# Performance work log

Hardware: AMD Instinct MI355X
Metric: run time of the kernel (lower is better)

The kernel has to match this reference:

```python
import jax, jax.numpy as jnp
import numpy as np

B, S, E = 1, 2048, 2048
H, KVH, D = 16, 4, 128  # query heads, kv heads, head dim (emb_kq == emb_v == 128)
SPLITS = (H * D, KVH * D, KVH * D)  # fused qkv output split sizes


def _rope_tables(seq_len, dim, base=10000.0):
    inv_freq = 1.0 / (base ** (jnp.arange(0, dim, 2, dtype=jnp.float32) / dim))
    t = jnp.arange(seq_len, dtype=jnp.float32)
    freqs = jnp.outer(t, inv_freq)  # [S, D/2]
    emb = jnp.concatenate([freqs, freqs], axis=-1)  # [S, D]
    return jnp.cos(emb), jnp.sin(emb)


def _rotate_half(x):
    x1, x2 = jnp.split(x, 2, axis=-1)
    return jnp.concatenate([-x2, x1], axis=-1)


def _apply_rope(x, cos, sin):
    # x: [B, S, h, D]; cos/sin: [S, D]
    c = cos[None, :, None, :]
    s = sin[None, :, None, :]
    return x * c + _rotate_half(x) * s


def setup_inputs() -> dict:
    key = jax.random.key(0)
    k1, k2, k3 = jax.random.split(key, 3)
    x = jax.random.normal(k1, (B, S, E), dtype=jnp.float32)
    w_qkv = jax.random.normal(k2, (sum(SPLITS), E), dtype=jnp.float32) * 0.02
    w_dense = jax.random.normal(k3, (E, H * D), dtype=jnp.float32) * 0.02
    return {"x": x, "w_qkv": w_qkv, "w_dense": w_dense}


def reference(x, w_qkv, w_dense):
    # fused QKV projection: [B, S, sum(SPLITS)]
    qkv = jnp.einsum("bse,fe->bsf", x, w_qkv)
    q, k, v = jnp.split(qkv, np.cumsum(SPLITS)[:-1].tolist(), axis=-1)
    q = q.reshape(B, S, H, D)
    k = k.reshape(B, S, KVH, D)
    v = v.reshape(B, S, KVH, D)

    # rotary position encoding on q, k
    cos, sin = _rope_tables(S, D)
    q = _apply_rope(q, cos, sin)
    k = _apply_rope(k, cos, sin)

    # GQA: expand kv heads to match query heads
    rep = H // KVH
    k = jnp.repeat(k, rep, axis=2)  # [B, S, H, D]
    v = jnp.repeat(v, rep, axis=2)

    # SDPA, causal
    scale = 1.0 / jnp.sqrt(jnp.asarray(D, dtype=x.dtype))
    scores = jnp.einsum("bqhd,bkhd->bhqk", q, k) * scale
    causal = jnp.tril(jnp.ones((S, S), dtype=bool))
    scores = jnp.where(causal[None, None], scores, jnp.asarray(-jnp.inf, scores.dtype))
    attn = jax.nn.softmax(scores, axis=-1)
    ctx = jnp.einsum("bhqk,bkhd->bqhd", attn, v).reshape(B, S, H * D)

    # output projection
    return jnp.einsum("bsf,ef->bse", ctx, w_dense)
```

## Files before the change

kernel.cpp:

```cpp
#include <hip/hip_runtime.h>
#include <hip/hip_bf16.h>
#include <math.h>

typedef __bf16 bf16;
typedef __bf16 bf16x4 __attribute__((ext_vector_type(4)));
typedef __bf16 bf16x8 __attribute__((ext_vector_type(8)));
typedef float  f32x4  __attribute__((ext_vector_type(4)));
typedef float  f32x16 __attribute__((ext_vector_type(16)));

#define S_LEN 2048
#define EMB   2048
#define NH    16
#define NKV   4
#define HD    128
#define FQKV  3072

__device__ __forceinline__ f32x4 mfma16(bf16x8 a, bf16x8 b, f32x4 c) {
  return __builtin_amdgcn_mfma_f32_16x16x32_bf16(a, b, c, 0, 0, 0);
}
__device__ __forceinline__ f32x16 mfma32(bf16x8 a, bf16x8 b, f32x16 c) {
  return __builtin_amdgcn_mfma_f32_32x32x16_bf16(a, b, c, 0, 0, 0);
}
__device__ __forceinline__ f32x16 zero16() {
  f32x16 v;
#pragma unroll
  for (int i = 0; i < 16; ++i) v[i] = 0.f;
  return v;
}

__global__ void cvt3_kernel(const float* __restrict__ a, bf16* __restrict__ ab, int na4,
                            const float* __restrict__ b, bf16* __restrict__ bb, int nb4,
                            const float* __restrict__ c, bf16* __restrict__ cb, int nc4,
                            float2* __restrict__ rt) {
  const int gid = blockIdx.x * blockDim.x + threadIdx.x;
  const int stride = gridDim.x * blockDim.x;
  const int total = na4 + nb4 + nc4;
  for (int i = gid; i < total; i += stride) {
    const float* src; bf16* dst; int j = i;
    if (j < na4)            { src = a; dst = ab; }
    else if (j < na4 + nb4) { j -= na4; src = b; dst = bb; }
    else                    { j -= na4 + nb4; src = c; dst = cb; }
    float4 v = reinterpret_cast<const float4*>(src)[j];
    bf16x4 o;
    o[0] = (bf16)v.x; o[1] = (bf16)v.y; o[2] = (bf16)v.z; o[3] = (bf16)v.w;
    reinterpret_cast<bf16x4*>(dst)[j] = o;
  }
  for (int i = gid; i < S_LEN * 64; i += stride) {
    const int spos = i >> 6, f = i & 63;
    const float inv = exp2f(-(float)f * (13.287712379549449f / 64.0f));
    float s, cc;
    sincosf((float)spos * inv, &s, &cc);
    rt[i] = make_float2(cc, s);
  }
}

template<int BM, int BN>
__global__ __launch_bounds__(256, ((BM == 64 && BN == 64) ? 4 : (BM == 64 ? 3 : 2)))
void gemm_bt(
    const bf16* __restrict__ A, const bf16* __restrict__ B,
    int M, int N, int K, int mode,
    bf16* __restrict__ qb, bf16* __restrict__ kb, bf16* __restrict__ vtb,
    float* __restrict__ outf, const float2* __restrict__ rt)
{
  constexpr int NFR = BN / 16;
  constexpr int MR  = BM / 4;
  constexpr int MT  = MR / 16;
  __shared__ __align__(16) bf16 As[BM * 64];
  __shared__ __align__(16) bf16 Bs[BN * 64];
  const int tid = threadIdx.x;
  const int w  = tid >> 6;
  const int l  = tid & 63;
  const int li = l & 15, lh = l >> 4;
  const int m0 = blockIdx.y * BM, n0 = blockIdx.x * BN;

  f32x4 acc[MT][NFR];
#pragma unroll
  for (int i = 0; i < MT; ++i)
#pragma unroll
    for (int j = 0; j < NFR; ++j) acc[i][j] = f32x4{0.f, 0.f, 0.f, 0.f};

  const int srow = l >> 3;
  const int schk = l & 7;

  for (int k0 = 0; k0 < K; k0 += 64) {
#pragma unroll
    for (int i = 0; i < BM / 32; ++i) {
      const int row = i * 32 + w * 8 + srow;
      const int sch = schk ^ (row & 7);
      const bf16* ga = A + (size_t)(m0 + row) * K + (k0 + sch * 8);
      bf16* la = As + (i * 32 + w * 8) * 64;
      __builtin_amdgcn_global_load_lds((const __attribute__((address_space(1))) void*)ga,
                                       (__attribute__((address_space(3))) void*)la, 16, 0, 0);
    }
#pragma unroll
    for (int i = 0; i < BN / 32; ++i) {
      const int row = i * 32 + w * 8 + srow;
      const int sch = schk ^ (row & 7);
      const bf16* gb = B + (size_t)(n0 + row) * K + (k0 + sch * 8);
      bf16* lb = Bs + (i * 32 + w * 8) * 64;
      __builtin_amdgcn_global_load_lds((const __attribute__((address_space(1))) void*)gb,
                                       (__attribute__((address_space(3))) void*)lb, 16, 0, 0);
    }
    __syncthreads();
#pragma unroll
    for (int kc = 0; kc < 2; ++kc) {
      bf16x8 afr[MT], bfr[NFR];
#pragma unroll
      for (int mt = 0; mt < MT; ++mt) {
        const int mr = w * MR + mt * 16 + li;
        const int c  = (kc * 4 + lh) ^ (mr & 7);
        afr[mt] = *reinterpret_cast<const bf16x8*>((const char*)As + mr * 128 + c * 16);
      }
#pragma unroll
      for (int nt = 0; nt < NFR; ++nt) {
        const int nr = nt * 16 + li;
        const int c  = (kc * 4 + lh) ^ (nr & 7);
        bfr[nt] = *reinterpret_cast<const bf16x8*>((const char*)Bs + nr * 128 + c * 16);
      }
#pragma unroll
      for (int mt = 0; mt < MT; ++mt)
#pragma unroll
        for (int nt = 0; nt < NFR; ++nt)
          acc[mt][nt] = mfma16(afr[mt], bfr[nt], acc[mt][nt]);
    }
    __syncthreads();
  }

  if (mode == 1) {
#pragma unroll
    for (int mt = 0; mt < MT; ++mt)
#pragma unroll
      for (int nt = 0; nt < NFR; ++nt)
#pragma unroll
        for (int r = 0; r < 4; ++r) {
          const int sr = m0 + w * MR + mt * 16 + lh * 4 + r;
          const int sc = n0 + nt * 16 + li;
          outf[(size_t)sr * N + sc] = acc[mt][nt][r];
        }
  } else {
    int seg, hh;
    if (n0 < NH * HD)             { seg = 0; hh = n0 >> 7; }
    else if (n0 < (NH + NKV) * HD){ seg = 1; hh = (n0 - NH * HD) >> 7; }
    else                          { seg = 2; hh = (n0 - (NH + NKV) * HD) >> 7; }

    if (seg == 2) {
#pragma unroll
      for (int mt = 0; mt < MT; ++mt) {
        const int S0 = m0 + w * MR + mt * 16 + lh * 4;
        const int T  = S0 >> 5;
        const int qp = (S0 & 31) >> 2;
        const int jj = (qp >> 2) & 1, hiv = qp & 1, ebase = 4 * ((qp >> 1) & 1);
        bf16* vdst = vtb + (size_t)hh * S_LEN * HD + (size_t)T * 4096;
#pragma unroll
        for (int nt = 0; nt < 8; ++nt) {
          const int dt = nt >> 1;
          const int lqv = (nt & 1) * 16 + li;
          bf16x4 pk;
#pragma unroll
          for (int r = 0; r < 4; ++r) pk[r] = (bf16)acc[mt][nt][r];
          *reinterpret_cast<bf16x4*>(
              vdst + ((dt * 2 + jj) * 2 + hiv) * 256 + lqv * 8 + ebase) = pk;
        }
      }
    } else {
      bf16* dstb = (seg == 0) ? (qb + (size_t)hh * S_LEN * HD)
                              : (kb + (size_t)hh * S_LEN * HD);
      const float qscale = (seg == 0) ? 0.08838834764831845f : 1.0f;
      const int hi2 = li >> 3, e2 = li & 7;
#pragma unroll
      for (int mt = 0; mt < MT; ++mt)
#pragma unroll
        for (int r = 0; r < 4; ++r) {
          const int spos = m0 + w * MR + mt * 16 + lh * 4 + r;
          const int T    = spos >> 5;
          const int lqr  = spos & 31;
          bf16* dst = dstb + (size_t)T * 4096;
          float cs[4], sn[4];
#pragma unroll
          for (int j = 0; j < 4; ++j) {
            const float2 t = rt[spos * 64 + j * 16 + li];
            cs[j] = t.x; sn[j] = t.y;
          }
#pragma unroll
          for (int nt = 0; nt < 8; ++nt) {
            const int j = nt & 3;
            const float x = acc[mt][nt][r];
            const float prt = acc[mt][nt ^ 4][r];
            const float rot = (nt < 4) ? -prt : prt;
            const float y = (x * cs[j] + rot * sn[j]) * qscale;
            dst[(nt * 2 + hi2) * 256 + lqr * 8 + e2] = (bf16)y;
          }
        }
    }
  }
}

__global__ __launch_bounds__(128, 2) void attn_kernel(
    const bf16* __restrict__ qb, const bf16* __restrict__ kb, const bf16* __restrict__ vtb,
    bf16* __restrict__ ctx)
{
  __shared__ __align__(16) char smem[32768];

  const int tid = threadIdx.x;
  const int ws = tid >> 6;
  const int l  = tid & 63;
  const int lq = l & 31;
  const int hi = l >> 5;
  const int b  = (int)blockIdx.x;
  const int layer = b >> 8, idx = b & 255;
  const int h    = idx & 15;
  const int base = idx >> 4;
  const int qt   = (layer == 0) ? (63 - base)
                 : (layer == 1) ? (32 + base)
                 : (layer == 2) ? (31 - base) : base;
  const int q0 = qt * 32;
  const int kh = h >> 2;

  bf16* Kbuf = (bf16*)(smem + ws * 16384);
  bf16* Vbuf = (bf16*)(smem + ws * 16384 + 8192);
  float* Obf = (float*)smem;

  const bf16* Qh = qb + (size_t)h * S_LEN * HD;
  const bf16* Kh = kb + (size_t)kh * S_LEN * HD;
  const bf16* Vh = vtb + (size_t)kh * S_LEN * HD;

  const float L2E = 1.4426950408889634f;
  const float BIG = -3.0e38f;

  const bf16* qtile = Qh + (size_t)qt * 4096;
  bf16x8 qfr[8];
#pragma unroll
  for (int kc = 0; kc < 8; ++kc)
    qfr[kc] = *reinterpret_cast<const bf16x8*>(qtile + (kc * 2 + hi) * 256 + lq * 8);

  f32x16 o[4];
#pragma unroll
  for (int dt = 0; dt < 4; ++dt) o[dt] = zero16();
  float lrow = 0.f;

  if (ws <= qt) {
    const bf16* ksrc = Kh + (size_t)ws * 4096 + l * 8;
    const bf16* vsrc = Vh + (size_t)ws * 4096 + l * 8;
#pragma unroll
    for (int c = 0; c < 8; ++c)
      __builtin_amdgcn_global_load_lds(
          (const __attribute__((address_space(1))) void*)(ksrc + c * 512),
          (__attribute__((address_space(3))) void*)(Kbuf + c * 512), 16, 0, 0);
#pragma unroll
    for (int c = 0; c < 8; ++c)
      __builtin_amdgcn_global_load_lds(
          (const __attribute__((address_space(1))) void*)(vsrc + c * 512),
          (__attribute__((address_space(3))) void*)(Vbuf + c * 512), 16, 0, 0);
  }

  for (int t = ws; t <= qt; t += 2) {
    const int tn = (t + 2 <= qt) ? (t + 2) : qt;
    asm volatile("s_waitcnt vmcnt(8)" ::: "memory");
    __builtin_amdgcn_sched_barrier(0);
    bf16x8 kf[8];
#pragma unroll
    for (int kc = 0; kc < 8; ++kc)
      kf[kc] = *reinterpret_cast<const bf16x8*>(Kbuf + (kc * 2 + hi) * 256 + lq * 8);
    asm volatile("s_waitcnt lgkmcnt(0)" ::: "memory");
    __builtin_amdgcn_sched_barrier(0);
    {
      const bf16* ksrc = Kh + (size_t)tn * 4096 + l * 8;
#pragma unroll
      for (int c = 0; c < 8; ++c)
        __builtin_amdgcn_global_load_lds(
            (const __attribute__((address_space(1))) void*)(ksrc + c * 512),
            (__attribute__((address_space(3))) void*)(Kbuf + c * 512), 16, 0, 0);
    }
    f32x16 sa = zero16(), sb = zero16();
    __builtin_amdgcn_s_setprio(1);
#pragma unroll
    for (int kc = 0; kc < 4; ++kc) {
      sa = mfma32(kf[kc], qfr[kc], sa);
      sb = mfma32(kf[kc + 4], qfr[kc + 4], sb);
    }
    __builtin_amdgcn_s_setprio(0);
    f32x16 s = sa + sb;
    asm volatile("s_waitcnt vmcnt(8)" ::: "memory");
    __builtin_amdgcn_sched_barrier(0);
    bf16x8 va[8];
#pragma unroll
    for (int sv = 0; sv < 8; ++sv)
      va[sv] = *reinterpret_cast<const bf16x8*>(Vbuf + (sv * 2 + hi) * 256 + lq * 8);
    asm volatile("s_waitcnt lgkmcnt(0)" ::: "memory");
    __builtin_amdgcn_sched_barrier(0);
    {
      const bf16* vsrc = Vh + (size_t)tn * 4096 + l * 8;
#pragma unroll
      for (int c = 0; c < 8; ++c)
        __builtin_amdgcn_global_load_lds(
            (const __attribute__((address_space(1))) void*)(vsrc + c * 512),
            (__attribute__((address_space(3))) void*)(Vbuf + c * 512), 16, 0, 0);
    }
    if (t == qt) {
      const int q = q0 + lq;
#pragma unroll
      for (int r = 0; r < 16; ++r) {
        const int kvv = (r & 3) + 8 * (r >> 2) + 4 * hi;
        if (t * 32 + kvv > q) s[r] = BIG;
      }
    }
    bf16x8 pb0, pb1;
    float tsum = 0.f;
#pragma unroll
    for (int r = 0; r < 8; ++r) {
      const float pv = exp2f(s[r] * L2E);
      tsum += pv; pb0[r] = (bf16)pv;
    }
#pragma unroll
    for (int r = 0; r < 8; ++r) {
      const float pv = exp2f(s[8 + r] * L2E);
      tsum += pv; pb1[r] = (bf16)pv;
    }
    tsum += __shfl_xor(tsum, 32);
    lrow += tsum;
    __builtin_amdgcn_s_setprio(1);
#pragma unroll
    for (int dt = 0; dt < 4; ++dt) {
      o[dt] = mfma32(va[2 * dt], pb0, o[dt]);
      o[dt] = mfma32(va[2 * dt + 1], pb1, o[dt]);
    }
    __builtin_amdgcn_s_setprio(0);
  }

  if (hi == 0) ((float*)(smem + ws * 16384 + 16128))[lq] = lrow;
  __syncthreads();
  float lgv = 0.f;
  if (ws == 0)
    lgv = ((float*)(smem + 16128))[lq] + ((float*)(smem + 16384 + 16128))[lq];
  __builtin_amdgcn_sched_barrier(0);
  if (ws == 0) {
#pragma unroll
    for (int dt = 0; dt < 4; ++dt)
#pragma unroll
      for (int r = 0; r < 16; ++r) {
        const int d = dt * 32 + (r & 3) + 8 * (r >> 2) + 4 * hi;
        Obf[lq * 129 + d] = o[dt][r];
      }
    if (hi == 0) ((float*)(smem + 16512))[lq] = lgv;
  }
  __syncthreads();
  if (ws == 1) {
#pragma unroll
    for (int dt = 0; dt < 4; ++dt)
#pragma unroll
      for (int r = 0; r < 16; ++r) {
        const int d = dt * 32 + (r & 3) + 8 * (r >> 2) + 4 * hi;
        Obf[lq * 129 + d] += o[dt][r];
      }
  }
  __syncthreads();
  {
    const int row = tid >> 2;
    const int d0 = (tid & 3) * 32;
    const float linv = 1.0f / ((float*)(smem + 16512))[row];
    const float* orow = Obf + row * 129 + d0;
    bf16* dst = ctx + (size_t)(q0 + row) * (NH * HD) + h * HD + d0;
#pragma unroll
    for (int j = 0; j < 4; ++j) {
      bf16x8 pk;
#pragma unroll
      for (int e = 0; e < 8; ++e) pk[e] = (bf16)(orow[j * 8 + e] * linv);
      *reinterpret_cast<bf16x8*>(dst + j * 8) = pk;
    }
  }
}

extern "C" void kernel_launch(void* const* d_in, const int* in_sizes, int n_in,
                              void* d_out, int out_size, void* d_ws, size_t ws_size,
                              hipStream_t stream)
{
  const float* x       = (const float*)d_in[0];
  const float* w_qkv   = (const float*)d_in[1];
  const float* w_dense = (const float*)d_in[2];
  float* out = (float*)d_out;

  char* ws = (char*)d_ws;
  size_t off = 0;
  bf16* xb    = (bf16*)(ws + off); off += (size_t)S_LEN * EMB * 2;
  bf16* wqkvb = (bf16*)(ws + off); off += (size_t)FQKV * EMB * 2;
  bf16* wdb   = (bf16*)(ws + off); off += (size_t)EMB * EMB * 2;
  bf16* qbuf  = (bf16*)(ws + off); off += (size_t)NH  * S_LEN * HD * 2;
  bf16* kbuf  = (bf16*)(ws + off); off += (size_t)NKV * S_LEN * HD * 2;
  bf16* vfbuf = (bf16*)(ws + off); off += (size_t)NKV * HD * S_LEN * 2;
  bf16* ctxb  = (bf16*)(ws + off); off += (size_t)S_LEN * NH * HD * 2;
  float2* rtab = (float2*)(ws + off); off += (size_t)S_LEN * 64 * sizeof(float2);
  (void)ws_size; (void)in_sizes; (void)n_in; (void)out_size;

  cvt3_kernel<<<2048, 256, 0, stream>>>(
      x, xb, S_LEN * EMB / 4,
      w_qkv, wqkvb, FQKV * EMB / 4,
      w_dense, wdb, EMB * EMB / 4, rtab);

  gemm_bt<64, 128><<<dim3(FQKV / 128, S_LEN / 64), 256, 0, stream>>>(
      xb, wqkvb, S_LEN, FQKV, EMB, 0, qbuf, kbuf, vfbuf, nullptr, rtab);

  attn_kernel<<<1024, 128, 0, stream>>>(qbuf, kbuf, vfbuf, ctxb);

  gemm_bt<64, 64><<<dim3(EMB / 64, S_LEN / 64), 256, 0, stream>>>(
      ctxb, wdb, S_LEN, EMB, NH * HD, 1, nullptr, nullptr, nullptr, out, rtab);
}
```

Baseline: 118.3 us.

## Process two query heads per attention block sharing K/V tiles across four waves

The attention kernel now assigns two query heads of the same KV group to each block, so every K/V tile loaded into LDS feeds MFMAs for both heads. The block grows to four waves that split the key tiles (stride 4), with partial outputs reduced serially through shared memory. This halves K/V global traffic per head and increases work per wave, but doubles accumulator registers (launch bounds 256,1), uses 64KB LDS, drops the balanced query-tile ordering for a simple descending order, and adds a longer serialized reduction.

```diff
diff --git a/kernel.cpp b/kernel.cpp
--- a/kernel.cpp
+++ b/kernel.cpp
@@ -195,52 +195,52 @@
   }
 }
 
-__global__ __launch_bounds__(128, 2) void attn_kernel(
+__global__ __launch_bounds__(256, 1) void attn_kernel(
     const bf16* __restrict__ qb, const bf16* __restrict__ kb, const bf16* __restrict__ vtb,
     bf16* __restrict__ ctx)
 {
-  __shared__ __align__(16) char smem[32768];
+  __shared__ __align__(16) char smem[65536];
 
   const int tid = threadIdx.x;
-  const int ws = tid >> 6;
+  const int w  = tid >> 6;
   const int l  = tid & 63;
   const int lq = l & 31;
   const int hi = l >> 5;
   const int b  = (int)blockIdx.x;
-  const int layer = b >> 8, idx = b & 255;
-  const int h    = idx & 15;
-  const int base = idx >> 4;
-  const int qt   = (layer == 0) ? (63 - base)
-                 : (layer == 1) ? (32 + base)
-                 : (layer == 2) ? (31 - base) : base;
+  const int qt = 63 - (b >> 3);
+  const int hp = b & 7;
+  const int h0 = hp * 2, h1 = h0 + 1;
   const int q0 = qt * 32;
-  const int kh = h >> 2;
-
-  bf16* Kbuf = (bf16*)(smem + ws * 16384);
-  bf16* Vbuf = (bf16*)(smem + ws * 16384 + 8192);
+  const int kh = hp >> 1;
+
+  bf16* Kbuf = (bf16*)(smem + w * 16384);
+  bf16* Vbuf = (bf16*)(smem + w * 16384 + 8192);
   float* Obf = (float*)smem;
-
-  const bf16* Qh = qb + (size_t)h * S_LEN * HD;
+  float* lpark = (float*)(smem + 49664);
+
   const bf16* Kh = kb + (size_t)kh * S_LEN * HD;
   const bf16* Vh = vtb + (size_t)kh * S_LEN * HD;
 
   const float L2E = 1.4426950408889634f;
   const float BIG = -3.0e38f;
 
-  const bf16* qtile = Qh + (size_t)qt * 4096;
-  bf16x8 qfr[8];
-#pragma unroll
-  for (int kc = 0; kc < 8; ++kc)
-    qfr[kc] = *reinterpret_cast<const bf16x8*>(qtile + (kc * 2 + hi) * 256 + lq * 8);
-
-  f32x16 o[4];
-#pragma unroll
-  for (int dt = 0; dt < 4; ++dt) o[dt] = zero16();
-  float lrow = 0.f;
-
-  if (ws <= qt) {
-    const bf16* ksrc = Kh + (size_t)ws * 4096 + l * 8;
-    const bf16* vsrc = Vh + (size_t)ws * 4096 + l * 8;
+  const bf16* qt0 = qb + (size_t)h0 * S_LEN * HD + (size_t)qt * 4096;
+  const bf16* qt1 = qb + (size_t)h1 * S_LEN * HD + (size_t)qt * 4096;
+  bf16x8 qfr0[8], qfr1[8];
+#pragma unroll
+  for (int kc = 0; kc < 8; ++kc) {
+    qfr0[kc] = *reinterpret_cast<const bf16x8*>(qt0 + (kc * 2 + hi) * 256 + lq * 8);
+    qfr1[kc] = *reinterpret_cast<const bf16x8*>(qt1 + (kc * 2 + hi) * 256 + lq * 8);
+  }
+
+  f32x16 o0[4], o1[4];
+#pragma unroll
+  for (int dt = 0; dt < 4; ++dt) { o0[dt] = zero16(); o1[dt] = zero16(); }
+  float l0 = 0.f, l1 = 0.f;
+
+  if (w <= qt) {
+    const bf16* ksrc = Kh + (size_t)w * 4096 + l * 8;
+    const bf16* vsrc = Vh + (size_t)w * 4096 + l * 8;
 #pragma unroll
     for (int c = 0; c < 8; ++c)
       __builtin_amdgcn_global_load_lds(
@@ -253,8 +253,8 @@
           (__attribute__((address_space(3))) void*)(Vbuf + c * 512), 16, 0, 0);
   }
 
-  for (int t = ws; t <= qt; t += 2) {
-    const int tn = (t + 2 <= qt) ? (t + 2) : qt;
+  for (int t = w; t <= qt; t += 4) {
+    const int tn = (t + 4 <= qt) ? (t + 4) : qt;
     asm volatile("s_waitcnt vmcnt(8)" ::: "memory");
     __builtin_amdgcn_sched_barrier(0);
     bf16x8 kf[8];
@@ -271,15 +271,29 @@
             (const __attribute__((address_space(1))) void*)(ksrc + c * 512),
             (__attribute__((address_space(3))) void*)(Kbuf + c * 512), 16, 0, 0);
     }
-    f32x16 sa = zero16(), sb = zero16();
-    __builtin_amdgcn_s_setprio(1);
-#pragma unroll
-    for (int kc = 0; kc < 4; ++kc) {
-      sa = mfma32(kf[kc], qfr[kc], sa);
-      sb = mfma32(kf[kc + 4], qfr[kc + 4], sb);
-    }
-    __builtin_amdgcn_s_setprio(0);
-    f32x16 s = sa + sb;
+    f32x16 s0, s1;
+    {
+      f32x16 sa = zero16(), sb = zero16();
+      __builtin_amdgcn_s_setprio(1);
+#pragma unroll
+      for (int kc = 0; kc < 4; ++kc) {
+        sa = mfma32(kf[kc], qfr0[kc], sa);
+        sb = mfma32(kf[kc + 4], qfr0[kc + 4], sb);
+      }
+      __builtin_amdgcn_s_setprio(0);
+      s0 = sa + sb;
+    }
+    {
+      f32x16 sa = zero16(), sb = zero16();
+      __builtin_amdgcn_s_setprio(1);
+#pragma unroll
+      for (int kc = 0; kc < 4; ++kc) {
+        sa = mfma32(kf[kc], qfr1[kc], sa);
+        sb = mfma32(kf[kc + 4], qfr1[kc + 4], sb);
+      }
+      __builtin_amdgcn_s_setprio(0);
+      s1 = sa + sb;
+    }
     asm volatile("s_waitcnt vmcnt(8)" ::: "memory");
     __builtin_amdgcn_sched_barrier(0);
     bf16x8 va[8];
@@ -301,72 +315,99 @@
 #pragma unroll
       for (int r = 0; r < 16; ++r) {
         const int kvv = (r & 3) + 8 * (r >> 2) + 4 * hi;
-        if (t * 32 + kvv > q) s[r] = BIG;
-      }
-    }
-    bf16x8 pb0, pb1;
-    float tsum = 0.f;
-#pragma unroll
-    for (int r = 0; r < 8; ++r) {
-      const float pv = exp2f(s[r] * L2E);
-      tsum += pv; pb0[r] = (bf16)pv;
-    }
-#pragma unroll
-    for (int r = 0; r < 8; ++r) {
-      const float pv = exp2f(s[8 + r] * L2E);
-      tsum += pv; pb1[r] = (bf16)pv;
-    }
-    tsum += __shfl_xor(tsum, 32);
-    lrow += tsum;
-    __builtin_amdgcn_s_setprio(1);
-#pragma unroll
-    for (int dt = 0; dt < 4; ++dt) {
-      o[dt] = mfma32(va[2 * dt], pb0, o[dt]);
-      o[dt] = mfma32(va[2 * dt + 1], pb1, o[dt]);
-    }
-    __builtin_amdgcn_s_setprio(0);
-  }
-
-  if (hi == 0) ((float*)(smem + ws * 16384 + 16128))[lq] = lrow;
+        if (t * 32 + kvv > q) { s0[r] = BIG; s1[r] = BIG; }
+      }
+    }
+    {
+      bf16x8 pb0, pb1;
+      float tsum = 0.f;
+#pragma unroll
+      for (int r = 0; r < 8; ++r) {
+        const float pv = exp2f(s0[r] * L2E);
+        tsum += pv; pb0[r] = (bf16)pv;
+      }
+#pragma unroll
+      for (int r = 0; r < 8; ++r) {
+        const float pv = exp2f(s0[8 + r] * L2E);
+        tsum += pv; pb1[r] = (bf16)pv;
+      }
+      tsum += __shfl_xor(tsum, 32);
+      l0 += tsum;
+      __builtin_amdgcn_s_setprio(1);
+#pragma unroll
+      for (int dt = 0; dt < 4; ++dt) {
+        o0[dt] = mfma32(va[2 * dt], pb0, o0[dt]);
+        o0[dt] = mfma32(va[2 * dt + 1], pb1, o0[dt]);
+      }
+      __builtin_amdgcn_s_setprio(0);
+    }
+    {
+      bf16x8 pb0, pb1;
+      float tsum = 0.f;
+#pragma unroll
+      for (int r = 0; r < 8; ++r) {
+        const float pv = exp2f(s1[r] * L2E);
+        tsum += pv; pb0[r] = (bf16)pv;
+      }
+#pragma unroll
+      for (int r = 0; r < 8; ++r) {
+        const float pv = exp2f(s1[8 + r] * L2E);
+        tsum += pv; pb1[r] = (bf16)pv;
+      }
+      tsum += __shfl_xor(tsum, 32);
+      l1 += tsum;
+      __builtin_amdgcn_s_setprio(1);
+#pragma unroll
+      for (int dt = 0; dt < 4; ++dt) {
+        o1[dt] = mfma32(va[2 * dt], pb0, o1[dt]);
+        o1[dt] = mfma32(va[2 * dt + 1], pb1, o1[dt]);
+      }
+      __builtin_amdgcn_s_setprio(0);
+    }
+  }
+
   __syncthreads();
-  float lgv = 0.f;
-  if (ws == 0)
-    lgv = ((float*)(smem + 16128))[lq] + ((float*)(smem + 16384 + 16128))[lq];
-  __builtin_amdgcn_sched_barrier(0);
-  if (ws == 0) {
-#pragma unroll
-    for (int dt = 0; dt < 4; ++dt)
-#pragma unroll
-      for (int r = 0; r < 16; ++r) {
-        const int d = dt * 32 + (r & 3) + 8 * (r >> 2) + 4 * hi;
-        Obf[lq * 129 + d] = o[dt][r];
-      }
-    if (hi == 0) ((float*)(smem + 16512))[lq] = lgv;
+  if (hi == 0) {
+    lpark[0 * 128 + w * 32 + lq] = l0;
+    lpark[1 * 128 + w * 32 + lq] = l1;
   }
   __syncthreads();
-  if (ws == 1) {
-#pragma unroll
-    for (int dt = 0; dt < 4; ++dt)
-#pragma unroll
-      for (int r = 0; r < 16; ++r) {
-        const int d = dt * 32 + (r & 3) + 8 * (r >> 2) + 4 * hi;
-        Obf[lq * 129 + d] += o[dt][r];
-      }
-  }
-  __syncthreads();
-  {
-    const int row = tid >> 2;
-    const int d0 = (tid & 3) * 32;
-    const float linv = 1.0f / ((float*)(smem + 16512))[row];
-    const float* orow = Obf + row * 129 + d0;
-    bf16* dst = ctx + (size_t)(q0 + row) * (NH * HD) + h * HD + d0;
-#pragma unroll
-    for (int j = 0; j < 4; ++j) {
-      bf16x8 pk;
-#pragma unroll
-      for (int e = 0; e < 8; ++e) pk[e] = (bf16)(orow[j * 8 + e] * linv);
-      *reinterpret_cast<bf16x8*>(dst + j * 8) = pk;
-    }
+
+#pragma unroll
+  for (int head = 0; head < 2; ++head) {
+    const f32x16* oh = head ? o1 : o0;
+#pragma unroll
+    for (int pass = 0; pass < 4; ++pass) {
+      if (w == pass) {
+#pragma unroll
+        for (int dt = 0; dt < 4; ++dt)
+#pragma unroll
+          for (int r = 0; r < 16; ++r) {
+            const int d = dt * 32 + (r & 3) + 8 * (r >> 2) + 4 * hi;
+            const float v = oh[dt][r];
+            if (pass == 0) Obf[lq * 129 + d] = v; else Obf[lq * 129 + d] += v;
+          }
+      }
+      __syncthreads();
+    }
+    {
+      const int row = tid >> 3;
+      const int d0 = (tid & 7) * 16;
+      const float lsum = lpark[head * 128 + 0 + row] + lpark[head * 128 + 32 + row]
+                       + lpark[head * 128 + 64 + row] + lpark[head * 128 + 96 + row];
+      const float linv = 1.0f / lsum;
+      const float* orow = Obf + row * 129 + d0;
+      bf16* dst = ctx + (size_t)(q0 + row) * (NH * HD) + (head ? h1 : h0) * HD + d0;
+      bf16x8 pk0, pk1;
+#pragma unroll
+      for (int e = 0; e < 8; ++e) {
+        pk0[e] = (bf16)(orow[e] * linv);
+        pk1[e] = (bf16)(orow[8 + e] * linv);
+      }
+      *reinterpret_cast<bf16x8*>(dst) = pk0;
+      *reinterpret_cast<bf16x8*>(dst + 8) = pk1;
+    }
+    __syncthreads();
   }
 }
 
@@ -399,7 +440,7 @@
   gemm_bt<64, 128><<<dim3(FQKV / 128, S_LEN / 64), 256, 0, stream>>>(
       xb, wqkvb, S_LEN, FQKV, EMB, 0, qbuf, kbuf, vfbuf, nullptr, rtab);
 
-  attn_kernel<<<1024, 128, 0, stream>>>(qbuf, kbuf, vfbuf, ctxb);
+  attn_kernel<<<512, 256, 0, stream>>>(qbuf, kbuf, vfbuf, ctxb);
 
   gemm_bt<64, 64><<<dim3(EMB / 64, S_LEN / 64), 256, 0, stream>>>(
       ctxb, wdb, S_LEN, EMB, NH * HD, 1, nullptr, nullptr, nullptr, out, rtab);
```

After: 123.6 us. 1.04x slower.
